# Kernel tuning notes

Measured on AMD Instinct MI355X. Metric: run time of the kernel, lower is better.

Reference implementation:

```python
import jax, jax.numpy as jnp
import numpy as np

NUM_GRAPHS = 64
NEG_SLOPE = 0.2


def _gatv2_conv(x, src, dst, Wl, bl, Wr, br, att, bias):
    # PyG GATv2Conv (concat=True, share_weights=False, residual=False)
    N = x.shape[0]
    H, C = att.shape
    xl = (x @ Wl.T + bl).reshape(N, H, C)  # source transform
    xr = (x @ Wr.T + br).reshape(N, H, C)  # target transform
    e = jax.nn.leaky_relu(xl[src] + xr[dst], NEG_SLOPE)      # [E,H,C]
    alpha = jnp.einsum('ehc,hc->eh', e, att)                 # [E,H]
    # softmax over incoming edges per target node (numerically stable)
    amax = jax.ops.segment_max(alpha, dst, num_segments=N)   # [N,H]
    amax = jnp.where(jnp.isfinite(amax), amax, 0.0)
    ex = jnp.exp(alpha - amax[dst])
    denom = jax.ops.segment_sum(ex, dst, num_segments=N)
    a = ex / (denom[dst] + 1e-16)                            # [E,H]
    out = jax.ops.segment_sum(xl[src] * a[:, :, None], dst, num_segments=N)  # [N,H,C]
    return out.reshape(N, H * C) + bias


def setup_inputs() -> dict:
    key = jax.random.key(0)
    ks = jax.random.split(key, 20)
    N, E, F_in, hidden, H = 50000, 1600000, 256, 128, 4
    C = hidden // H
    s = 0.05
    inp = {
        'x': jax.random.normal(ks[0], (N, F_in), dtype=jnp.float32),
        'edge_index': jax.random.randint(ks[1], (2, E), 0, N, dtype=jnp.int64),
        'batch': jnp.sort(jax.random.randint(ks[2], (N,), 0, NUM_GRAPHS, dtype=jnp.int64)),
        # layer 1 (in=F_in)
        'Wl1': jax.random.normal(ks[3], (hidden, F_in), dtype=jnp.float32) * s,
        'bl1': jnp.zeros((hidden,), dtype=jnp.float32),
        'Wr1': jax.random.normal(ks[4], (hidden, F_in), dtype=jnp.float32) * s,
        'br1': jnp.zeros((hidden,), dtype=jnp.float32),
        'att1': jax.random.normal(ks[5], (H, C), dtype=jnp.float32) * s,
        'bias1': jnp.zeros((hidden,), dtype=jnp.float32),
        # layer 2 (in=hidden)
        'Wl2': jax.random.normal(ks[6], (hidden, hidden), dtype=jnp.float32) * s,
        'bl2': jnp.zeros((hidden,), dtype=jnp.float32),
        'Wr2': jax.random.normal(ks[7], (hidden, hidden), dtype=jnp.float32) * s,
        'br2': jnp.zeros((hidden,), dtype=jnp.float32),
        'att2': jax.random.normal(ks[8], (H, C), dtype=jnp.float32) * s,
        'bias2': jnp.zeros((hidden,), dtype=jnp.float32),
        # head
        'Wlin': jax.random.normal(ks[9], (1, hidden), dtype=jnp.float32) * s,
        'blin': jnp.zeros((1,), dtype=jnp.float32),
    }
    return inp


def reference(x, edge_index, batch, Wl1, bl1, Wr1, br1, att1, bias1,
              Wl2, bl2, Wr2, br2, att2, bias2, Wlin, blin):
    N = x.shape[0]
    loop = jnp.arange(N, dtype=edge_index.dtype)
    src = jnp.concatenate([edge_index[0], loop])  # add_self_loops=True
    dst = jnp.concatenate([edge_index[1], loop])
    h = _gatv2_conv(x, src, dst, Wl1, bl1, Wr1, br1, att1, bias1)
    h = jax.nn.relu(h)  # norm=Identity, dropout no-op in eval
    h = _gatv2_conv(h, src, dst, Wl2, bl2, Wr2, br2, att2, bias2)
    # global_mean_pool
    sums = jax.ops.segment_sum(h, batch, num_segments=NUM_GRAPHS)
    cnt = jax.ops.segment_sum(jnp.ones((N,), h.dtype), batch, num_segments=NUM_GRAPHS)
    pooled = sums / jnp.maximum(cnt, 1.0)[:, None]
    return pooled @ Wlin.T + blin
```

## Files before the change

### kernel.cpp

```cpp
#include <hip/hip_runtime.h>
#include <hip/hip_fp16.h>
#include <math.h>
#include <stdint.h>

#define EPB 4096
#define NBKT 128

typedef _Float16 f16x8 __attribute__((ext_vector_type(8)));
typedef float f32x4 __attribute__((ext_vector_type(4)));
typedef float f32x2 __attribute__((ext_vector_type(2)));
typedef _Float16 h2 __attribute__((ext_vector_type(2)));

#define LOG2E 1.4426950f

__device__ __forceinline__ float fast_exp2(float x) {
#if __has_builtin(__builtin_amdgcn_exp2f)
    return __builtin_amdgcn_exp2f(x);
#else
    return __expf(x * 0.69314718f);
#endif
}

template<int CTRL>
__device__ __forceinline__ float dpp_add(float x) {
    union { float f; int i; } u, v;
    u.f = x;
    v.i = __builtin_amdgcn_update_dpp(0, u.i, CTRL, 0xF, 0xF, true);
    return x + v.f;
}
__device__ __forceinline__ float reduce16(float x) {
    x = dpp_add<0xB1>(x);
    x = dpp_add<0x4E>(x);
    x = dpp_add<0x124>(x);
    x = dpp_add<0x128>(x);
    return x;
}

__global__ void k_wpack_all(const float* __restrict__ Wl1, const float* __restrict__ Wr1,
                            const float* __restrict__ Wl2, const float* __restrict__ Wr2,
                            _Float16* __restrict__ Wp1, _Float16* __restrict__ Wp2,
                            int K1) {
    int t = blockIdx.x * 256 + threadIdx.x;
    int total1 = (K1 / 32) * 16 * 64;
    int total2 = (128 / 32) * 16 * 64;
    if (t < total1) {
        int l = t & 63, ct = (t >> 6) & 15, kt = t >> 10;
        int col = ct * 16 + (l & 15);
        int k0 = kt * 32 + (l >> 4) * 8;
        const float* src = (col < 128) ? (Wl1 + (size_t)col * K1)
                                       : (Wr1 + (size_t)(col - 128) * K1);
        union { _Float16 h[8]; uint4 u; } o;
#pragma unroll
        for (int e = 0; e < 8; ++e) o.h[e] = (_Float16)src[k0 + e];
        reinterpret_cast<uint4*>(Wp1)[t] = o.u;
    } else if (t < total1 + total2) {
        int t2 = t - total1;
        int l = t2 & 63, ct = (t2 >> 6) & 15, kt = t2 >> 10;
        int col = ct * 16 + (l & 15);
        int k0 = kt * 32 + (l >> 4) * 8;
        const float* src = (col < 128) ? (Wl2 + (size_t)col * 128)
                                       : (Wr2 + (size_t)(col - 128) * 128);
        union { _Float16 h[8]; uint4 u; } o;
#pragma unroll
        for (int e = 0; e < 8; ++e) {
            int k = k0 + e;
            int m = k >> 1, hh = m >> 4, j = m & 15;
            int c0 = hh * 32 + j;
            int chan = (k & 1) ? c0 + 16 : c0;
            o.h[e] = (_Float16)src[chan];
        }
        reinterpret_cast<uint4*>(Wp2)[t2] = o.u;
    }
}

template<int K, int CVT>
__global__ __launch_bounds__(256) void k_gemm_mfma(
    const void* __restrict__ Xin, const _Float16* __restrict__ Wp,
    const float* __restrict__ bl, const float* __restrict__ br,
    const float* __restrict__ att,
    uint32_t* __restrict__ xlh, float2* __restrict__ xrp,
    float* __restrict__ ledl, int N) {
    __shared__ _Float16 xs[64 * K];
    const int t = threadIdx.x, w = t >> 6, l = t & 63;
    const int row0 = blockIdx.x * 64;
    if (CVT) {
        const float* X = (const float*)Xin;
        for (int cid = t; cid < 64 * (K / 4); cid += 256) {
            int r = cid / (K / 4), c4 = (cid % (K / 4)) * 4;
            int gr = row0 + r;
            float4 v = make_float4(0.f, 0.f, 0.f, 0.f);
            if (gr < N) v = *reinterpret_cast<const float4*>(X + (size_t)gr * K + c4);
            h2 lo = {(_Float16)v.x, (_Float16)v.y};
            h2 hi = {(_Float16)v.z, (_Float16)v.w};
            uint2 pk;
            pk.x = __builtin_bit_cast(uint32_t, lo);
            pk.y = __builtin_bit_cast(uint32_t, hi);
            int ba = (r * K * 2 + c4 * 2) ^ ((r & 7) << 4);
            *reinterpret_cast<uint2*>(reinterpret_cast<char*>(xs) + ba) = pk;
        }
    } else {
        const _Float16* X = (const _Float16*)Xin;
        for (int cid = t; cid < 64 * (K / 8); cid += 256) {
            int r = cid / (K / 8), c8 = (cid % (K / 8)) * 8;
            int gr = row0 + r;
            uint4 v = make_uint4(0u, 0u, 0u, 0u);
            if (gr < N) v = *reinterpret_cast<const uint4*>(X + (size_t)gr * K + c8);
            int ba = (r * K * 2 + c8 * 2) ^ ((r & 7) << 4);
            *reinterpret_cast<uint4*>(reinterpret_cast<char*>(xs) + ba) = v;
        }
    }
    __syncthreads();
    f32x4 acc[4][4];
#pragma unroll
    for (int m = 0; m < 4; ++m)
#pragma unroll
        for (int n = 0; n < 4; ++n) acc[m][n] = (f32x4){0.f, 0.f, 0.f, 0.f};
#pragma unroll
    for (int kt = 0; kt < K / 32; ++kt) {
        f16x8 a[4], b[4];
#pragma unroll
        for (int m = 0; m < 4; ++m) {
            int r = m * 16 + (l & 15);
            int ba = (r * K * 2 + kt * 64 + (l >> 4) * 16) ^ ((r & 7) << 4);
            a[m] = *reinterpret_cast<const f16x8*>(reinterpret_cast<const char*>(xs) + ba);
        }
#pragma unroll
        for (int n = 0; n < 4; ++n) {
            int ct = w * 4 + n;
            b[n] = *reinterpret_cast<const f16x8*>(Wp + ((size_t)(kt * 16 + ct) * 64 + l) * 8);
        }
#pragma unroll
        for (int m = 0; m < 4; ++m)
#pragma unroll
            for (int n = 0; n < 4; ++n)
                acc[m][n] = __builtin_amdgcn_mfma_f32_16x16x32_f16(a[m], b[n], acc[m][n], 0, 0, 0);
    }
    const int j = l & 15;
    if (w < 2) {
        float attv[2][2], bv[2][2];
#pragma unroll
        for (int p = 0; p < 2; ++p) {
            int c0 = (2 * w + p) * 32 + j;
            attv[p][0] = att[c0]; attv[p][1] = att[c0 + 16];
            bv[p][0] = bl[c0];    bv[p][1] = bl[c0 + 16];
        }
#pragma unroll
        for (int m = 0; m < 4; ++m)
#pragma unroll
            for (int r4 = 0; r4 < 4; ++r4) {
                int gr = row0 + m * 16 + (l >> 4) * 4 + r4;
                bool ok = gr < N;
#pragma unroll
                for (int p = 0; p < 2; ++p) {
                    int h = 2 * w + p;
                    float v0 = acc[m][2 * p][r4] + bv[p][0];
                    float v1 = acc[m][2 * p + 1][r4] + bv[p][1];
                    float part = reduce16(fmaf(attv[p][0], v0, attv[p][1] * v1));
                    if (ok) {
                        h2 hp = {(_Float16)v0, (_Float16)v1};
                        xlh[(size_t)gr * 64 + h * 16 + j] = __builtin_bit_cast(uint32_t, hp);
                        if (j == 0) ledl[gr * 4 + h] = 0.6f * LOG2E * part;
                    }
                }
            }
    } else {
        float bv[2][2];
#pragma unroll
        for (int p = 0; p < 2; ++p) {
            int c0 = (2 * (w - 2) + p) * 32 + j;
            bv[p][0] = br[c0]; bv[p][1] = br[c0 + 16];
        }
#pragma unroll
        for (int m = 0; m < 4; ++m)
#pragma unroll
            for (int r4 = 0; r4 < 4; ++r4) {
                int gr = row0 + m * 16 + (l >> 4) * 4 + r4;
                if (gr < N) {
#pragma unroll
                    for (int p = 0; p < 2; ++p) {
                        int hh = 2 * (w - 2) + p;
                        float v0 = acc[m][2 * p][r4] + bv[p][0];
                        float v1 = acc[m][2 * p + 1][r4] + bv[p][1];
                        xrp[(size_t)gr * 64 + hh * 16 + j] = make_float2(v0, v1);
                    }
                }
            }
    }
}

__global__ __launch_bounds__(256) void k_hist(const int* __restrict__ dstArr,
                                              int* __restrict__ g_hist, int E,
                                              float* __restrict__ zbuf, int zn) {
    __shared__ int h[NBKT];
    int t = threadIdx.x;
    int zi = blockIdx.x * 256 + t;
    if (zi < zn) zbuf[zi] = 0.f;
    if (t < NBKT) h[t] = 0;
    __syncthreads();
    int s0 = blockIdx.x * EPB, s1 = min(E, s0 + EPB);
    for (int i = s0 + t; i < s1; i += 256) atomicAdd(&h[dstArr[i] >> 9], 1);
    __syncthreads();
    if (t < NBKT) g_hist[blockIdx.x * NBKT + t] = h[t];
}
__global__ __launch_bounds__(512) void k_part_scan(const int* __restrict__ g_hist,
                                                   int* __restrict__ g_base,
                                                   int* __restrict__ bstart_out,
                                                   int NB1, int E) {
    __shared__ int csum[4][NBKT];
    __shared__ int btot[NBKT];
    __shared__ int bstart[NBKT];
    int tid = threadIdx.x, c = tid >> 7, b = tid & (NBKT - 1);
    int chunk = (NB1 + 3) >> 2;
    int i0 = c * chunk, i1 = min(NB1, i0 + chunk);
    int run = 0;
    for (int i = i0; i < i1; ++i) run += g_hist[i * NBKT + b];
    csum[c][b] = run;
    __syncthreads();
    int mytot = 0;
    if (c == 0) {
        mytot = csum[0][b] + csum[1][b] + csum[2][b] + csum[3][b];
        btot[b] = mytot;
    }
    __syncthreads();
    for (int off = 1; off < NBKT; off <<= 1) {
        int add = 0;
        if (c == 0 && b >= off) add = btot[b - off];
        __syncthreads();
        if (c == 0) btot[b] += add;
        __syncthreads();
    }
    if (c == 0) { bstart[b] = btot[b] - mytot; bstart_out[b] = bstart[b]; }
    if (tid == 0) bstart_out[NBKT] = E;
    __syncthreads();
    int base = bstart[b];
    for (int cc = 0; cc < c; ++cc) base += csum[cc][b];
    run = base;
    for (int i = i0; i < i1; ++i) {
        g_base[i * NBKT + b] = run;
        run += g_hist[i * NBKT + b];
    }
}
__global__ __launch_bounds__(256) void k_scatter(const int* __restrict__ ei,
                                                 const int* __restrict__ g_base,
                                                 uint32_t* __restrict__ tmp, int E) {
    __shared__ int off[NBKT];
    int t = threadIdx.x;
    if (t < NBKT) off[t] = g_base[blockIdx.x * NBKT + t];
    __syncthreads();
    int s0 = blockIdx.x * EPB, s1 = min(E, s0 + EPB);
    for (int i = s0 + t; i < s1; i += 256) {
        int s = ei[i], d = ei[E + i];
        int pos = atomicAdd(&off[d >> 9], 1);
        tmp[pos] = ((uint32_t)s << 16) | (uint32_t)d;
    }
}
__global__ __launch_bounds__(256) void k_bucket_csr(
    const uint32_t* __restrict__ tmp, const int* __restrict__ bstart,
    int* __restrict__ rowptr, int* __restrict__ csr, int N, int E) {
    __shared__ int cnt[512];
    __shared__ int fil[512];
    int b = blockIdx.x, t = threadIdx.x;
    int s0 = bstart[b], s1 = bstart[b + 1];
    cnt[t] = 0; cnt[t + 256] = 0;
    __syncthreads();
    for (int i = s0 + t; i < s1; i += 256)
        atomicAdd(&cnt[tmp[i] & 511], 1);
    __syncthreads();
    int c0 = cnt[t], c1 = cnt[t + 256];
    for (int off = 1; off < 512; off <<= 1) {
        int v0 = (t >= off) ? cnt[t - off] : 0;
        int v1 = (t + 256 >= off) ? cnt[t + 256 - off] : 0;
        __syncthreads();
        cnt[t] += v0; cnt[t + 256] += v1;
        __syncthreads();
    }
    int e0 = cnt[t] - c0, e1 = cnt[t + 256] - c1;
    __syncthreads();
    cnt[t] = e0; cnt[t + 256] = e1;
    fil[t] = 1; fil[t + 256] = 1;
    __syncthreads();
    int n0 = b * 512;
#pragma unroll
    for (int k = 0; k < 2; ++k) {
        int ld = t + k * 256, n = n0 + ld;
        if (n < N) {
            int rp = s0 + cnt[ld] + n;
            rowptr[n] = rp;
            csr[rp] = n;
        }
    }
    if (b == 0 && t == 0) rowptr[N] = E + N;
    for (int i = s0 + t; i < s1; i += 256) {
        uint32_t pk = tmp[i];
        int d = (int)(pk & 0xFFFFu), ld = d & 511;
        int slot = atomicAdd(&fil[ld], 1);
        csr[s0 + cnt[ld] + d + slot] = (int)(pk >> 16);
    }
}

__device__ __forceinline__ void edge_compute(
    uint32_t q, float lv, f32x2 xr2, float a04, float a14,
    float& ssum, f32x2& acc2) {
    h2 A = __builtin_bit_cast(h2, q);
    f32x2 A2 = {(float)A.x, (float)A.y};
    f32x2 t2 = A2 + xr2;
    float p = fmaf(fabsf(t2.y), a14, fabsf(t2.x) * a04);
    p = reduce16(p);
    float w = fast_exp2(p + lv);
    ssum += w;
    acc2 = __builtin_elementwise_fma((f32x2){w, w}, A2, acc2);
}

template<int OUT16>
__global__ __launch_bounds__(256) void k_gat_edge(
    const uint32_t* __restrict__ xlh, const float2* __restrict__ xrp,
    const float* __restrict__ ledl, const float* __restrict__ att,
    const float* __restrict__ bias,
    const int* __restrict__ rowptr, const int* __restrict__ csr,
    void* __restrict__ out, int N) {
    const int l = threadIdx.x & 63;
    const int n = __builtin_amdgcn_readfirstlane(blockIdx.x * 4 + (threadIdx.x >> 6));
    if (n >= N) return;
    const int h = l >> 4, j = l & 15;
    const int c0 = h * 32 + j, c1 = c0 + 16;
    const float2 xrv = xrp[(size_t)n * 64 + l];
    const f32x2 xr2 = {xrv.x, xrv.y};
    const float a04 = att[c0] * (0.4f * LOG2E), a14 = att[c1] * (0.4f * LOG2E);
    f32x2 acc2 = {0.f, 0.f};
    float ssum = 0.f;
    const int beg = rowptr[n], end = rowptr[n + 1];
    int i = beg;
    if (i + 7 < end) {
        uint32_t q0[8]; float lv0[8];
#pragma unroll
        for (int e = 0; e < 8; ++e) {
            int s = __builtin_amdgcn_readfirstlane(csr[i + e]);
            q0[e]  = xlh[(size_t)(uint32_t)s * 64 + l];
            lv0[e] = ledl[(uint32_t)s * 4 + h];
        }
        for (; i + 15 < end; i += 8) {
            uint32_t q1[8]; float lv1[8];
#pragma unroll
            for (int e = 0; e < 8; ++e) {
                int s = __builtin_amdgcn_readfirstlane(csr[i + 8 + e]);
                q1[e]  = xlh[(size_t)(uint32_t)s * 64 + l];
                lv1[e] = ledl[(uint32_t)s * 4 + h];
            }
#pragma unroll
            for (int e = 0; e < 8; ++e)
                edge_compute(q0[e], lv0[e], xr2, a04, a14, ssum, acc2);
#pragma unroll
            for (int e = 0; e < 8; ++e) { q0[e] = q1[e]; lv0[e] = lv1[e]; }
        }
#pragma unroll
        for (int e = 0; e < 8; ++e)
            edge_compute(q0[e], lv0[e], xr2, a04, a14, ssum, acc2);
        i += 8;
    }
    for (; i < end; ++i) {
        int s = __builtin_amdgcn_readfirstlane(csr[i]);
        uint32_t q = xlh[(size_t)(uint32_t)s * 64 + l];
        float lv  = ledl[(uint32_t)s * 4 + h];
        edge_compute(q, lv, xr2, a04, a14, ssum, acc2);
    }
    float inv = 1.f / ssum;
    float o0 = fmaf(acc2.x, inv, bias[c0]);
    float o1 = fmaf(acc2.y, inv, bias[c1]);
    if (OUT16) {
        o0 = fmaxf(o0, 0.f); o1 = fmaxf(o1, 0.f);
        h2 oh = {(_Float16)o0, (_Float16)o1};
        ((uint32_t*)out)[(size_t)n * 64 + l] = __builtin_bit_cast(uint32_t, oh);
    } else {
        ((float2*)out)[(size_t)n * 64 + l] = make_float2(o0, o1);
    }
}

__global__ __launch_bounds__(128) void k_pool(
    const float* __restrict__ h, const int* __restrict__ batch,
    float* __restrict__ pool, float* __restrict__ gcnt, int N) {
    const int NPB = 32;
    int c = threadIdx.x;
    int n0 = blockIdx.x * NPB;
    int n1 = min(n0 + NPB, N);
    float acc = 0.f;
    int curg = -1, cntl = 0;
    for (int n = n0; n < n1; ++n) {
        int g = batch[n];
        if (g != curg) {
            if (curg >= 0) {
                atomicAdd(&pool[curg * 128 + c], acc);
                if (c == 0) atomicAdd(&gcnt[curg], (float)cntl);
            }
            acc = 0.f; cntl = 0; curg = g;
        }
        acc += h[(size_t)n * 128 + c];
        cntl++;
    }
    if (curg >= 0) {
        atomicAdd(&pool[curg * 128 + c], acc);
        if (c == 0) atomicAdd(&gcnt[curg], (float)cntl);
    }
}
__global__ __launch_bounds__(64) void k_head(
    const float* __restrict__ pool, const float* __restrict__ gcnt,
    const float* __restrict__ Wlin, const float* __restrict__ blin,
    float* __restrict__ out, int G) {
    int g = blockIdx.x, l = threadIdx.x;
    float2 pv = ((const float2*)pool)[g * 64 + l];
    int c0 = (l >> 4) * 32 + (l & 15);
    float d = pv.x * Wlin[c0] + pv.y * Wlin[c0 + 16];
#pragma unroll
    for (int off = 32; off; off >>= 1) d += __shfl_xor(d, off, 64);
    if (l == 0) {
        float cnt = fmaxf(gcnt[g], 1.f);
        out[g] = d / cnt + blin[0];
    }
}

extern "C" void kernel_launch(void* const* d_in, const int* in_sizes, int n_in,
                              void* d_out, int out_size, void* d_ws, size_t ws_size,
                              hipStream_t stream) {
    const float* x     = (const float*)d_in[0];
    const int*   ei    = (const int*)d_in[1];
    const int*   batch = (const int*)d_in[2];
    const float* Wl1   = (const float*)d_in[3];
    const float* bl1   = (const float*)d_in[4];
    const float* Wr1   = (const float*)d_in[5];
    const float* br1   = (const float*)d_in[6];
    const float* att1  = (const float*)d_in[7];
    const float* bias1 = (const float*)d_in[8];
    const float* Wl2   = (const float*)d_in[9];
    const float* bl2   = (const float*)d_in[10];
    const float* Wr2   = (const float*)d_in[11];
    const float* br2   = (const float*)d_in[12];
    const float* att2  = (const float*)d_in[13];
    const float* bias2 = (const float*)d_in[14];
    const float* Wlin  = (const float*)d_in[15];
    const float* blin  = (const float*)d_in[16];

    const int N   = in_sizes[2];
    const int E   = in_sizes[1] / 2;
    const int Fin = in_sizes[0] / N;
    const int G   = out_size;
    (void)n_in; (void)ws_size;

    char* p = (char*)d_ws;
    auto alloc = [&](size_t bytes) -> char* {
        char* r = p;
        p += (bytes + 255) & ~(size_t)255;
        return r;
    };
    uint32_t* xlh   = (uint32_t*)alloc((size_t)N * 64 * 4);
    float2*   xrp   = (float2*)alloc((size_t)N * 64 * 8);
    uint32_t* hbh   = (uint32_t*)alloc((size_t)N * 64 * 4);
    float*    hbf   = (float*)alloc((size_t)N * 128 * 4);
    float*    ledl  = (float*)alloc((size_t)N * 4 * 4);
    float*    wt1   = (float*)alloc((size_t)Fin * 256 * 2);
    float*    wt2   = (float*)alloc((size_t)128 * 256 * 2);
    int*      rowptr= (int*)alloc((size_t)(N + 1) * 4);
    int*      csr   = (int*)alloc((size_t)(E + N) * 4);
    float*    poolg = (float*)alloc((size_t)G * 129 * 4);
    float*    pool  = poolg;
    float*    gcnt  = poolg + (size_t)G * 128;

    const int NB1 = (E + EPB - 1) / EPB;
    int*      g_hist = (int*)alloc((size_t)NB1 * NBKT * 4);
    int*      g_base = (int*)alloc((size_t)NB1 * NBKT * 4);
    int*      bstart = (int*)alloc((size_t)(NBKT + 1) * 4);
    uint32_t* tmp = (uint32_t*)xrp;
    _Float16* Wp1 = (_Float16*)wt1;
    _Float16* Wp2 = (_Float16*)wt2;

    const int wb = (N + 3) / 4;
    const int gb = (N + 63) / 64;

    k_hist<<<NB1, 256, 0, stream>>>(ei + E, g_hist, E, poolg, G * 129);
    k_part_scan<<<1, 512, 0, stream>>>(g_hist, g_base, bstart, NB1, E);
    k_scatter<<<NB1, 256, 0, stream>>>(ei, g_base, tmp, E);
    k_bucket_csr<<<NBKT, 256, 0, stream>>>(tmp, bstart, rowptr, csr, N, E);

    {
        int total = (Fin / 32) * 16 * 64 + (128 / 32) * 16 * 64;
        k_wpack_all<<<(total + 255) / 256, 256, 0, stream>>>(Wl1, Wr1, Wl2, Wr2, Wp1, Wp2, Fin);
    }

    k_gemm_mfma<256, 1><<<gb, 256, 0, stream>>>(x, Wp1, bl1, br1, att1, xlh, xrp, ledl, N);
    k_gat_edge<1><<<wb, 256, 0, stream>>>(xlh, xrp, ledl, att1, bias1, rowptr, csr, hbh, N);

    k_gemm_mfma<128, 0><<<gb, 256, 0, stream>>>(hbh, Wp2, bl2, br2, att2, xlh, xrp, ledl, N);
    k_gat_edge<0><<<wb, 256, 0, stream>>>(xlh, xrp, ledl, att2, bias2, rowptr, csr, hbf, N);

    k_pool<<<(N + 31) / 32, 128, 0, stream>>>(hbf, batch, pool, gcnt, N);
    k_head<<<G, 64, 0, stream>>>(pool, gcnt, Wlin, blin, (float*)d_out, G);
}
```

Baseline: 287.6 us.

## Halve GEMM row tile to 32 and drop software pipelining in edge loop

The projection GEMM kernel now handles 32 rows per block instead of 64, which halves shared memory and accumulator registers and doubles the grid. The intent is higher occupancy and more blocks in flight, at the cost of reloading the packed weights twice as often. The GAT edge kernel's double-buffered prefetch of 8 edges is replaced by a simple batch loop that loads 8 neighbors and then computes them. This cuts register pressure but removes the overlap of the next batch's gathers with the current compute.

```diff
diff --git a/kernel.cpp b/kernel.cpp
--- a/kernel.cpp
+++ b/kernel.cpp
@@ -80,12 +80,12 @@
     const float* __restrict__ att,
     uint32_t* __restrict__ xlh, float2* __restrict__ xrp,
     float* __restrict__ ledl, int N) {
-    __shared__ _Float16 xs[64 * K];
+    __shared__ _Float16 xs[32 * K];
     const int t = threadIdx.x, w = t >> 6, l = t & 63;
-    const int row0 = blockIdx.x * 64;
+    const int row0 = blockIdx.x * 32;
     if (CVT) {
         const float* X = (const float*)Xin;
-        for (int cid = t; cid < 64 * (K / 4); cid += 256) {
+        for (int cid = t; cid < 32 * (K / 4); cid += 256) {
             int r = cid / (K / 4), c4 = (cid % (K / 4)) * 4;
             int gr = row0 + r;
             float4 v = make_float4(0.f, 0.f, 0.f, 0.f);
@@ -100,7 +100,7 @@
         }
     } else {
         const _Float16* X = (const _Float16*)Xin;
-        for (int cid = t; cid < 64 * (K / 8); cid += 256) {
+        for (int cid = t; cid < 32 * (K / 8); cid += 256) {
             int r = cid / (K / 8), c8 = (cid % (K / 8)) * 8;
             int gr = row0 + r;
             uint4 v = make_uint4(0u, 0u, 0u, 0u);
@@ -110,16 +110,16 @@
         }
     }
     __syncthreads();
-    f32x4 acc[4][4];
-#pragma unroll
-    for (int m = 0; m < 4; ++m)
+    f32x4 acc[2][4];
+#pragma unroll
+    for (int m = 0; m < 2; ++m)
 #pragma unroll
         for (int n = 0; n < 4; ++n) acc[m][n] = (f32x4){0.f, 0.f, 0.f, 0.f};
 #pragma unroll
     for (int kt = 0; kt < K / 32; ++kt) {
-        f16x8 a[4], b[4];
-#pragma unroll
-        for (int m = 0; m < 4; ++m) {
+        f16x8 a[2], b[4];
+#pragma unroll
+        for (int m = 0; m < 2; ++m) {
             int r = m * 16 + (l & 15);
             int ba = (r * K * 2 + kt * 64 + (l >> 4) * 16) ^ ((r & 7) << 4);
             a[m] = *reinterpret_cast<const f16x8*>(reinterpret_cast<const char*>(xs) + ba);
@@ -130,7 +130,7 @@
             b[n] = *reinterpret_cast<const f16x8*>(Wp + ((size_t)(kt * 16 + ct) * 64 + l) * 8);
         }
 #pragma unroll
-        for (int m = 0; m < 4; ++m)
+        for (int m = 0; m < 2; ++m)
 #pragma unroll
             for (int n = 0; n < 4; ++n)
                 acc[m][n] = __builtin_amdgcn_mfma_f32_16x16x32_f16(a[m], b[n], acc[m][n], 0, 0, 0);
@@ -145,7 +145,7 @@
             bv[p][0] = bl[c0];    bv[p][1] = bl[c0 + 16];
         }
 #pragma unroll
-        for (int m = 0; m < 4; ++m)
+        for (int m = 0; m < 2; ++m)
 #pragma unroll
             for (int r4 = 0; r4 < 4; ++r4) {
                 int gr = row0 + m * 16 + (l >> 4) * 4 + r4;
@@ -171,7 +171,7 @@
             bv[p][0] = br[c0]; bv[p][1] = br[c0 + 16];
         }
 #pragma unroll
-        for (int m = 0; m < 4; ++m)
+        for (int m = 0; m < 2; ++m)
 #pragma unroll
             for (int r4 = 0; r4 < 4; ++r4) {
                 int gr = row0 + m * 16 + (l >> 4) * 4 + r4;
@@ -296,19 +296,6 @@
         int slot = atomicAdd(&fil[ld], 1);
         csr[s0 + cnt[ld] + d + slot] = (int)(pk >> 16);
     }
-}
-
-__device__ __forceinline__ void edge_compute(
-    uint32_t q, float lv, f32x2 xr2, float a04, float a14,
-    float& ssum, f32x2& acc2) {
-    h2 A = __builtin_bit_cast(h2, q);
-    f32x2 A2 = {(float)A.x, (float)A.y};
-    f32x2 t2 = A2 + xr2;
-    float p = fmaf(fabsf(t2.y), a14, fabsf(t2.x) * a04);
-    p = reduce16(p);
-    float w = fast_exp2(p + lv);
-    ssum += w;
-    acc2 = __builtin_elementwise_fma((f32x2){w, w}, A2, acc2);
 }
 
 template<int OUT16>
@@ -330,38 +317,40 @@
     float ssum = 0.f;
     const int beg = rowptr[n], end = rowptr[n + 1];
     int i = beg;
-    if (i + 7 < end) {
-        uint32_t q0[8]; float lv0[8];
+    for (; i + 7 < end; i += 8) {
+        int sr[8];
+#pragma unroll
+        for (int e = 0; e < 8; ++e) sr[e] = __builtin_amdgcn_readfirstlane(csr[i + e]);
+        uint32_t q[8]; float lv[8];
 #pragma unroll
         for (int e = 0; e < 8; ++e) {
-            int s = __builtin_amdgcn_readfirstlane(csr[i + e]);
-            q0[e]  = xlh[(size_t)(uint32_t)s * 64 + l];
-            lv0[e] = ledl[(uint32_t)s * 4 + h];
-        }
-        for (; i + 15 < end; i += 8) {
-            uint32_t q1[8]; float lv1[8];
-#pragma unroll
-            for (int e = 0; e < 8; ++e) {
-                int s = __builtin_amdgcn_readfirstlane(csr[i + 8 + e]);
-                q1[e]  = xlh[(size_t)(uint32_t)s * 64 + l];
-                lv1[e] = ledl[(uint32_t)s * 4 + h];
-            }
-#pragma unroll
-            for (int e = 0; e < 8; ++e)
-                edge_compute(q0[e], lv0[e], xr2, a04, a14, ssum, acc2);
-#pragma unroll
-            for (int e = 0; e < 8; ++e) { q0[e] = q1[e]; lv0[e] = lv1[e]; }
-        }
-#pragma unroll
-        for (int e = 0; e < 8; ++e)
-            edge_compute(q0[e], lv0[e], xr2, a04, a14, ssum, acc2);
-        i += 8;
+            q[e]  = xlh[(size_t)(uint32_t)sr[e] * 64 + l];
+            lv[e] = ledl[(uint32_t)sr[e] * 4 + h];
+        }
+#pragma unroll
+        for (int e = 0; e < 8; ++e) {
+            h2 A = __builtin_bit_cast(h2, q[e]);
+            f32x2 A2 = {(float)A.x, (float)A.y};
+            f32x2 t2 = A2 + xr2;
+            float p = fmaf(fabsf(t2.y), a14, fabsf(t2.x) * a04);
+            p = reduce16(p);
+            float w = fast_exp2(p + lv[e]);
+            ssum += w;
+            acc2 = __builtin_elementwise_fma((f32x2){w, w}, A2, acc2);
+        }
     }
     for (; i < end; ++i) {
         int s = __builtin_amdgcn_readfirstlane(csr[i]);
         uint32_t q = xlh[(size_t)(uint32_t)s * 64 + l];
         float lv  = ledl[(uint32_t)s * 4 + h];
-        edge_compute(q, lv, xr2, a04, a14, ssum, acc2);
+        h2 A = __builtin_bit_cast(h2, q);
+        f32x2 A2 = {(float)A.x, (float)A.y};
+        f32x2 t2 = A2 + xr2;
+        float p = fmaf(fabsf(t2.y), a14, fabsf(t2.x) * a04);
+        p = reduce16(p);
+        float w = fast_exp2(p + lv);
+        ssum += w;
+        acc2 = __builtin_elementwise_fma((f32x2){w, w}, A2, acc2);
     }
     float inv = 1.f / ssum;
     float o0 = fmaf(acc2.x, inv, bias[c0]);
@@ -472,7 +461,7 @@
     _Float16* Wp2 = (_Float16*)wt2;
 
     const int wb = (N + 3) / 4;
-    const int gb = (N + 63) / 64;
+    const int gb = (N + 31) / 32;
 
     k_hist<<<NB1, 256, 0, stream>>>(ei + E, g_hist, E, poolg, G * 129);
     k_part_scan<<<1, 512, 0, stream>>>(g_hist, g_base, bstart, NB1, E);
```

Measured after the change: 272.9 us. 1.05x faster.
